# Optimization experiments

Measured on AMD Instinct MI355X. Metric: run time of the kernel, lower is better.

## Reference

```python
import jax, jax.numpy as jnp
import numpy as np

D_MODEL = 1024
STATE_DIM = 64
SEQ_L = 2048


def hippo_legs_A(N):
    n = jnp.arange(N, dtype=jnp.float32)
    two_n1 = 2.0 * n + 1.0
    sq = jnp.sqrt(two_n1[:, None] * two_n1[None, :])
    A = jnp.tril(sq, k=-1) * -1.0
    return A + jnp.diag(-(n + 1.0))


def setup_inputs() -> dict:
    key = jax.random.key(0)
    kB, kC = jax.random.split(key)
    N = STATE_DIM
    n = jnp.arange(N, dtype=jnp.float32)
    B_ref = jnp.sqrt(2.0 * n + 1.0)  # (N,)
    B = jnp.tile(B_ref[None, :], (D_MODEL, 1)) + 0.01 * jax.random.normal(kB, (D_MODEL, N), dtype=jnp.float32)
    C = 0.1 * jax.random.normal(kC, (D_MODEL, N), dtype=jnp.float32)
    D = jnp.zeros((D_MODEL,), dtype=jnp.float32)
    log_dt = jnp.log(jnp.asarray(0.1, dtype=jnp.float32))
    return {"B": B, "C": C, "D": D, "log_dt": log_dt, "L": SEQ_L}


def reference(B, C, D, log_dt, L):
    N = B.shape[1]
    A = hippo_legs_A(N)                       # (N,N) continuous-time HiPPO-LegS
    dt = jax.nn.softplus(log_dt) + 1e-06
    I = jnp.eye(N, dtype=A.dtype)
    lhs = I - 0.5 * dt * A
    rhs = I + 0.5 * dt * A
    A_bar = jnp.linalg.solve(lhs, rhs)        # (N,N) bilinear discretization
    B_bar = jnp.linalg.solve(lhs, (dt * B).T).T  # (d_model, N)
    A_bar_T = A_bar.T

    def step(x, _):
        y = jnp.sum(C * x, axis=-1)           # (d_model,)
        return x @ A_bar_T, y

    _, ys = jax.lax.scan(step, B_bar, None, length=L)  # ys: (L, d_model)
    K = ys.T                                   # (d_model, L)
    K = K.at[:, 0].add(D)
    return K[:, None, :]                       # (d_model, 1, L)
```

## Files before the change

kernel.cpp:

```cpp
#include <hip/hip_runtime.h>

namespace {

template<int CTRL, int RM>
__device__ __forceinline__ float dpp_mov0(float v) {
  return __int_as_float(__builtin_amdgcn_update_dpp(
      0, __float_as_int(v), CTRL, RM, 0xF, false));
}
template<int CTRL, int RM>
__device__ __forceinline__ float dpp_mov1(float v) {
  return __int_as_float(__builtin_amdgcn_update_dpp(
      0x3f800000, __float_as_int(v), CTRL, RM, 0xF, false));
}

struct Hoist {
  float cs0, cs1, cs2, cs3, cs4, cs5;
  float gs0, gs1, gs2, gs3, gs4, gs5;
  float r, inv_d, hr, alpha, k2;
};

__device__ __forceinline__ Hoist make_hoist(float dt, int n) {
  float h = 0.5f * dt, fn = (float)n;
  float r = sqrtf(2.f * fn + 1.f);
  float d = 1.f + h * (fn + 1.f);
  float inv_d = 1.f / d;
  float g = (1.f - h * fn) * inv_d;
  float c = g - 1.f;
  Hoist H;
  H.r = r; H.inv_d = inv_d; H.hr = h * r;
  H.alpha = 1.f + h * fn;
  H.k2 = r * (2.f - d) * inv_d;
#define COEF_STEP(IDX, CTRL, RM)                                        \
  H.cs##IDX = c; H.gs##IDX = g;                                         \
  { float cP = dpp_mov0<CTRL, RM>(c);                                   \
    float gP = dpp_mov1<CTRL, RM>(g);                                   \
    c = fmaf(g, cP, c); g = g * gP; }
  COEF_STEP(0, 0x111, 0xF)
  COEF_STEP(1, 0x112, 0xF)
  COEF_STEP(2, 0x114, 0xF)
  COEF_STEP(3, 0x118, 0xF)
  COEF_STEP(4, 0x142, 0xA)
  COEF_STEP(5, 0x143, 0xC)
#undef COEF_STEP
  return H;
}

__device__ __forceinline__ float abar_apply(float x, const Hoist& H) {
  float w1 = H.r * x, w2 = H.k2 * x;
#define APPLY_STEP(IDX, CTRL, RM)                                       \
  { float w1P = dpp_mov0<CTRL, RM>(w1);                                 \
    float w2P = dpp_mov0<CTRL, RM>(w2);                                 \
    w2 = fmaf(H.cs##IDX, w1P, fmaf(H.gs##IDX, w2P, w2));                \
    w1 += w1P; }
  APPLY_STEP(0, 0x111, 0xF)
  APPLY_STEP(1, 0x112, 0xF)
  APPLY_STEP(2, 0x114, 0xF)
  APPLY_STEP(3, 0x118, 0xF)
  APPLY_STEP(4, 0x142, 0xA)
  APPLY_STEP(5, 0x143, 0xC)
#undef APPLY_STEP
  float tp = dpp_mov0<0x138, 0xF>(w2);
  return H.inv_d * fmaf(-H.hr, w1 + tp, H.alpha * x);
}

template<int CTRL, int RM>
__device__ __forceinline__ void linrec_step(float& G, float& W) {
  float Wo = dpp_mov0<CTRL, RM>(W);
  float Go = dpp_mov1<CTRL, RM>(G);
  W = fmaf(G, Wo, W);
  G *= Go;
}
__device__ __forceinline__ float lhs_solve(float z, const Hoist& H) {
  float G = H.gs0, W = H.r * z * H.inv_d;
  linrec_step<0x111, 0xF>(G, W);
  linrec_step<0x112, 0xF>(G, W);
  linrec_step<0x114, 0xF>(G, W);
  linrec_step<0x118, 0xF>(G, W);
  linrec_step<0x142, 0xA>(G, W);
  linrec_step<0x143, 0xC>(G, W);
  float sp = dpp_mov0<0x138, 0xF>(W);
  return (z - H.hr * sp) * H.inv_d;
}

__device__ __forceinline__ float softplus_dt(float ldt) {
  return log1pf(expf(ldt)) + 1e-6f;
}

__device__ __forceinline__ void load_row(const float* __restrict__ base,
                                         float (&pc)[64]) {
  const float4* p4 = (const float4*)base;
  #pragma unroll
  for (int q = 0; q < 16; ++q) {
    float4 f = p4[q];
    pc[4*q+0] = f.x; pc[4*q+1] = f.y; pc[4*q+2] = f.z; pc[4*q+3] = f.w;
  }
}

__device__ __forceinline__ float qapply(const float (&pc)[64], float u) {
  float a0 = 0.f, a1 = 0.f, a2 = 0.f, a3 = 0.f;
  #pragma unroll
  for (int k = 0; k < 64; k += 4) {
    float u0 = __int_as_float(__builtin_amdgcn_readlane(__float_as_int(u), k + 0));
    float u1 = __int_as_float(__builtin_amdgcn_readlane(__float_as_int(u), k + 1));
    float u2 = __int_as_float(__builtin_amdgcn_readlane(__float_as_int(u), k + 2));
    float u3 = __int_as_float(__builtin_amdgcn_readlane(__float_as_int(u), k + 3));
    a0 = fmaf(pc[k + 0], u0, a0);
    a1 = fmaf(pc[k + 1], u1, a1);
    a2 = fmaf(pc[k + 2], u2, a2);
    a3 = fmaf(pc[k + 3], u3, a3);
  }
  return (a0 + a1) + (a2 + a3);
}

__device__ __forceinline__ float lds_matvec(const float (&pc)[64],
                                            const float* row) {
  const float4* r4 = (const float4*)row;
  float a0 = 0.f, a1 = 0.f, a2 = 0.f, a3 = 0.f;
  #pragma unroll
  for (int q = 0; q < 16; ++q) {
    float4 f = r4[q];
    a0 = fmaf(pc[4*q+0], f.x, a0);
    a1 = fmaf(pc[4*q+1], f.y, a1);
    a2 = fmaf(pc[4*q+2], f.z, a2);
    a3 = fmaf(pc[4*q+3], f.w, a3);
  }
  return (a0 + a1) + (a2 + a3);
}

}

__global__ __launch_bounds__(64) void hippo_pow(const float* __restrict__ ldt_p,
                                                float* __restrict__ A32c,
                                                float* __restrict__ QROW,
                                                float* __restrict__ Q2ROW) {
  const int lane = threadIdx.x;
  const int m = blockIdx.x;
  const float dt = softplus_dt(ldt_p[0]);
  const Hoist H = make_hoist(dt, lane);
  float x = (lane == m) ? 1.f : 0.f;
  #pragma unroll 1
  for (int s = 0; s < 32; ++s) x = abar_apply(x, H);
  A32c[lane * 64 + m] = x;
  #pragma unroll 1
  for (int s = 0; s < 32; ++s) x = abar_apply(x, H);
  QROW[m * 64 + lane] = x;
  #pragma unroll 1
  for (int s = 0; s < 64; ++s) x = abar_apply(x, H);
  Q2ROW[m * 64 + lane] = x;
}

__global__ __launch_bounds__(256, 4) void hippo_main(
    const float* __restrict__ B, const float* __restrict__ C,
    const float* __restrict__ Dv, const float* __restrict__ ldt_p,
    const float* __restrict__ A32c, const float* __restrict__ QROW,
    const float* __restrict__ Q2ROW, float* __restrict__ out, int NI, int L) {
  __shared__ __align__(16) float Vl[64 * 65];
  __shared__ __align__(16) float Ul[32 * 64];
  const int d = blockIdx.x;
  const int tau = threadIdx.x;
  const int lane = tau & 63;
  const int w = tau >> 6;
  const float dt = softplus_dt(ldt_p[0]);
  const Hoist H = make_hoist(dt, lane);

  if (w == 0) {
    float v = lhs_solve(dt * B[d * 64 + lane], H);
    #pragma unroll 1
    for (int j = 0; j < 32; ++j) {
      Vl[j * 65 + lane] = v;
      if (j < 31) v = abar_apply(v, H);
    }
  } else if (w == 3) {
    float bb = lhs_solve(dt * B[d * 64 + lane], H);
    float pc[64];
    load_row(A32c + lane * 64, pc);
    float v = qapply(pc, bb);
    #pragma unroll 1
    for (int j = 32; j < 64; ++j) {
      Vl[j * 65 + lane] = v;
      if (j < 63) v = abar_apply(v, H);
    }
  } else if (w == 1) {
    float pc[64];
    load_row(Q2ROW + lane * 64, pc);
    float u = C[d * 64 + lane];
    const int nE = (NI + 1) >> 1;
    #pragma unroll 1
    for (int a = 0; a < nE; ++a) {
      Ul[(2 * a) * 64 + lane] = u;
      if (a < nE - 1) u = lds_matvec(pc, Ul + (2 * a) * 64);
    }
  } else {
    float pc[64];
    load_row(QROW + lane * 64, pc);
    float u = qapply(pc, C[d * 64 + lane]);
    load_row(Q2ROW + lane * 64, pc);
    const int nO = NI >> 1;
    #pragma unroll 1
    for (int a = 0; a < nO; ++a) {
      Ul[(2 * a + 1) * 64 + lane] = u;
      if (a < nO - 1) u = lds_matvec(pc, Ul + (2 * a + 1) * 64);
    }
  }
  __syncthreads();

  const int j = lane;
  float vr[64];
  #pragma unroll
  for (int n = 0; n < 64; ++n) vr[n] = Vl[j * 65 + n];
  #pragma unroll
  for (int k = 0; k < 8; ++k) {
    const int i = w + 4 * k;
    if (i < NI) {
      const float4* u4 = (const float4*)(Ul + i * 64);
      float a0 = 0.f, a1 = 0.f, a2 = 0.f, a3 = 0.f;
      #pragma unroll
      for (int q = 0; q < 16; ++q) {
        float4 f = u4[q];
        a0 = fmaf(vr[4*q+0], f.x, a0);
        a1 = fmaf(vr[4*q+1], f.y, a1);
        a2 = fmaf(vr[4*q+2], f.z, a2);
        a3 = fmaf(vr[4*q+3], f.w, a3);
      }
      float y = (a0 + a1) + (a2 + a3);
      if ((i | j) == 0) y += Dv[d];
      out[(size_t)d * L + i * 64 + j] = y;
    }
  }
}

extern "C" void kernel_launch(void* const* d_in, const int* in_sizes, int n_in,
                              void* d_out, int out_size, void* d_ws, size_t ws_size,
                              hipStream_t stream) {
  const float* B   = (const float*)d_in[0];
  const float* C   = (const float*)d_in[1];
  const float* Dv  = (const float*)d_in[2];
  const float* ldt = (const float*)d_in[3];
  const int d_model = in_sizes[2];
  const int L = out_size / d_model;
  const int NI = L / 64;
  float* A32c  = (float*)d_ws;
  float* QROW  = (float*)d_ws + 4096;
  float* Q2ROW = (float*)d_ws + 8192;
  hippo_pow<<<64, 64, 0, stream>>>(ldt, A32c, QROW, Q2ROW);
  hippo_main<<<d_model, 256, 0, stream>>>(B, C, Dv, ldt, A32c, QROW, Q2ROW,
                                          (float*)d_out, NI, L);
}
```

Before: 44.79 us.

## Cut register pressure in hippo_main by streaming matrices from LDS and global memory

Replaces the 64-register row caches (pc[64], vr[64]) with on-the-fly matvecs: the A32c and QROW products read rows from global memory and broadcast the input with readlane. The Q2 recurrence now reads a transposed copy staged in shared memory. The final V·U contraction is split into four 16-wide chunks with per-output accumulators. V storage switches from 65-column padding to an XOR swizzle. The aim is lower VGPR use so the 4-blocks-per-CU launch bound holds without spills, at the cost of extra LDS traffic per recurrence step, a serial accumulation order, and a larger shared footprint.

```diff
diff --git a/kernel.cpp b/kernel.cpp
--- a/kernel.cpp
+++ b/kernel.cpp
@@ -11,6 +11,10 @@
 __device__ __forceinline__ float dpp_mov1(float v) {
   return __int_as_float(__builtin_amdgcn_update_dpp(
       0x3f800000, __float_as_int(v), CTRL, RM, 0xF, false));
+}
+
+__device__ __forceinline__ float rl(float v, int k) {
+  return __int_as_float(__builtin_amdgcn_readlane(__float_as_int(v), k));
 }
 
 struct Hoist {
@@ -86,43 +90,33 @@
   return log1pf(expf(ldt)) + 1e-6f;
 }
 
-__device__ __forceinline__ void load_row(const float* __restrict__ base,
-                                         float (&pc)[64]) {
-  const float4* p4 = (const float4*)base;
+__device__ __forceinline__ float grow_matvec(const float* __restrict__ M,
+                                             float u, int lane) {
+  float a0 = 0.f, a1 = 0.f, a2 = 0.f, a3 = 0.f;
+  const float4* m4 = (const float4*)(M + lane * 64);
   #pragma unroll
   for (int q = 0; q < 16; ++q) {
-    float4 f = p4[q];
-    pc[4*q+0] = f.x; pc[4*q+1] = f.y; pc[4*q+2] = f.z; pc[4*q+3] = f.w;
-  }
-}
-
-__device__ __forceinline__ float qapply(const float (&pc)[64], float u) {
+    float4 f = m4[q];
+    a0 = fmaf(f.x, rl(u, 4 * q + 0), a0);
+    a1 = fmaf(f.y, rl(u, 4 * q + 1), a1);
+    a2 = fmaf(f.z, rl(u, 4 * q + 2), a2);
+    a3 = fmaf(f.w, rl(u, 4 * q + 3), a3);
+  }
+  return (a0 + a1) + (a2 + a3);
+}
+
+__device__ __forceinline__ float q2t_matvec(const float* Q2T, float u, int lane) {
   float a0 = 0.f, a1 = 0.f, a2 = 0.f, a3 = 0.f;
   #pragma unroll
   for (int k = 0; k < 64; k += 4) {
-    float u0 = __int_as_float(__builtin_amdgcn_readlane(__float_as_int(u), k + 0));
-    float u1 = __int_as_float(__builtin_amdgcn_readlane(__float_as_int(u), k + 1));
-    float u2 = __int_as_float(__builtin_amdgcn_readlane(__float_as_int(u), k + 2));
-    float u3 = __int_as_float(__builtin_amdgcn_readlane(__float_as_int(u), k + 3));
-    a0 = fmaf(pc[k + 0], u0, a0);
-    a1 = fmaf(pc[k + 1], u1, a1);
-    a2 = fmaf(pc[k + 2], u2, a2);
-    a3 = fmaf(pc[k + 3], u3, a3);
-  }
-  return (a0 + a1) + (a2 + a3);
-}
-
-__device__ __forceinline__ float lds_matvec(const float (&pc)[64],
-                                            const float* row) {
-  const float4* r4 = (const float4*)row;
-  float a0 = 0.f, a1 = 0.f, a2 = 0.f, a3 = 0.f;
-  #pragma unroll
-  for (int q = 0; q < 16; ++q) {
-    float4 f = r4[q];
-    a0 = fmaf(pc[4*q+0], f.x, a0);
-    a1 = fmaf(pc[4*q+1], f.y, a1);
-    a2 = fmaf(pc[4*q+2], f.z, a2);
-    a3 = fmaf(pc[4*q+3], f.w, a3);
+    float q0 = Q2T[(k + 0) * 64 + lane];
+    float q1 = Q2T[(k + 1) * 64 + lane];
+    float q2 = Q2T[(k + 2) * 64 + lane];
+    float q3 = Q2T[(k + 3) * 64 + lane];
+    a0 = fmaf(q0, rl(u, k + 0), a0);
+    a1 = fmaf(q1, rl(u, k + 1), a1);
+    a2 = fmaf(q2, rl(u, k + 2), a2);
+    a3 = fmaf(q3, rl(u, k + 3), a3);
   }
   return (a0 + a1) + (a2 + a3);
 }
@@ -154,75 +148,100 @@
     const float* __restrict__ Dv, const float* __restrict__ ldt_p,
     const float* __restrict__ A32c, const float* __restrict__ QROW,
     const float* __restrict__ Q2ROW, float* __restrict__ out, int NI, int L) {
-  __shared__ __align__(16) float Vl[64 * 65];
+  __shared__ __align__(16) float Vl[64 * 64];
   __shared__ __align__(16) float Ul[32 * 64];
+  __shared__ __align__(16) float Q2T[64 * 64];
   const int d = blockIdx.x;
   const int tau = threadIdx.x;
   const int lane = tau & 63;
   const int w = tau >> 6;
-  const float dt = softplus_dt(ldt_p[0]);
-  const Hoist H = make_hoist(dt, lane);
 
   if (w == 0) {
-    float v = lhs_solve(dt * B[d * 64 + lane], H);
+    const Hoist H = make_hoist(softplus_dt(ldt_p[0]), lane);
+    float v = lhs_solve(softplus_dt(ldt_p[0]) * B[d * 64 + lane], H);
     #pragma unroll 1
     for (int j = 0; j < 32; ++j) {
-      Vl[j * 65 + lane] = v;
+      Vl[j * 64 + (lane ^ (j & 31))] = v;
       if (j < 31) v = abar_apply(v, H);
     }
   } else if (w == 3) {
-    float bb = lhs_solve(dt * B[d * 64 + lane], H);
-    float pc[64];
-    load_row(A32c + lane * 64, pc);
-    float v = qapply(pc, bb);
+    const Hoist H = make_hoist(softplus_dt(ldt_p[0]), lane);
+    float bb = lhs_solve(softplus_dt(ldt_p[0]) * B[d * 64 + lane], H);
+    float v = grow_matvec(A32c, bb, lane);
     #pragma unroll 1
     for (int j = 32; j < 64; ++j) {
-      Vl[j * 65 + lane] = v;
+      Vl[j * 64 + (lane ^ (j & 31))] = v;
       if (j < 63) v = abar_apply(v, H);
     }
-  } else if (w == 1) {
-    float pc[64];
-    load_row(Q2ROW + lane * 64, pc);
-    float u = C[d * 64 + lane];
-    const int nE = (NI + 1) >> 1;
-    #pragma unroll 1
-    for (int a = 0; a < nE; ++a) {
-      Ul[(2 * a) * 64 + lane] = u;
-      if (a < nE - 1) u = lds_matvec(pc, Ul + (2 * a) * 64);
-    }
   } else {
-    float pc[64];
-    load_row(QROW + lane * 64, pc);
-    float u = qapply(pc, C[d * 64 + lane]);
-    load_row(Q2ROW + lane * 64, pc);
-    const int nO = NI >> 1;
-    #pragma unroll 1
-    for (int a = 0; a < nO; ++a) {
-      Ul[(2 * a + 1) * 64 + lane] = u;
-      if (a < nO - 1) u = lds_matvec(pc, Ul + (2 * a + 1) * 64);
+    #pragma unroll
+    for (int q = 0; q < 16; ++q) {
+      float4 f = *(const float4*)(Q2ROW + lane * 64 + 4 * q);
+      Q2T[(4 * q + 0) * 64 + lane] = f.x;
+      Q2T[(4 * q + 1) * 64 + lane] = f.y;
+      Q2T[(4 * q + 2) * 64 + lane] = f.z;
+      Q2T[(4 * q + 3) * 64 + lane] = f.w;
+    }
+    if (w == 1) {
+      float u = C[d * 64 + lane];
+      const int nE = (NI + 1) >> 1;
+      #pragma unroll 1
+      for (int a = 0; a < nE; ++a) {
+        Ul[(2 * a) * 64 + lane] = u;
+        if (a < nE - 1) u = q2t_matvec(Q2T, u, lane);
+      }
+    } else {
+      float u = grow_matvec(QROW, C[d * 64 + lane], lane);
+      const int nO = NI >> 1;
+      #pragma unroll 1
+      for (int a = 0; a < nO; ++a) {
+        Ul[(2 * a + 1) * 64 + lane] = u;
+        if (a < nO - 1) u = q2t_matvec(Q2T, u, lane);
+      }
     }
   }
   __syncthreads();
 
   const int j = lane;
-  float vr[64];
-  #pragma unroll
-  for (int n = 0; n < 64; ++n) vr[n] = Vl[j * 65 + n];
+  float acc[8];
+  #pragma unroll
+  for (int k = 0; k < 8; ++k) acc[k] = 0.f;
+  #pragma unroll
+  for (int h = 0; h < 4; ++h) {
+    float vr[16];
+    #pragma unroll
+    for (int e = 0; e < 16; ++e)
+      vr[e] = Vl[j * 64 + ((16 * h + e) ^ (j & 31))];
+    #pragma unroll
+    for (int k = 0; k < 8; ++k) {
+      const int i = w + 4 * k;
+      if (i < NI) {
+        const float4* u4 = (const float4*)(Ul + i * 64 + 16 * h);
+        float4 f0 = u4[0], f1 = u4[1], f2 = u4[2], f3 = u4[3];
+        acc[k] = fmaf(vr[0],  f0.x, acc[k]);
+        acc[k] = fmaf(vr[1],  f0.y, acc[k]);
+        acc[k] = fmaf(vr[2],  f0.z, acc[k]);
+        acc[k] = fmaf(vr[3],  f0.w, acc[k]);
+        acc[k] = fmaf(vr[4],  f1.x, acc[k]);
+        acc[k] = fmaf(vr[5],  f1.y, acc[k]);
+        acc[k] = fmaf(vr[6],  f1.z, acc[k]);
+        acc[k] = fmaf(vr[7],  f1.w, acc[k]);
+        acc[k] = fmaf(vr[8],  f2.x, acc[k]);
+        acc[k] = fmaf(vr[9],  f2.y, acc[k]);
+        acc[k] = fmaf(vr[10], f2.z, acc[k]);
+        acc[k] = fmaf(vr[11], f2.w, acc[k]);
+        acc[k] = fmaf(vr[12], f3.x, acc[k]);
+        acc[k] = fmaf(vr[13], f3.y, acc[k]);
+        acc[k] = fmaf(vr[14], f3.z, acc[k]);
+        acc[k] = fmaf(vr[15], f3.w, acc[k]);
+      }
+    }
+  }
   #pragma unroll
   for (int k = 0; k < 8; ++k) {
     const int i = w + 4 * k;
     if (i < NI) {
-      const float4* u4 = (const float4*)(Ul + i * 64);
-      float a0 = 0.f, a1 = 0.f, a2 = 0.f, a3 = 0.f;
-      #pragma unroll
-      for (int q = 0; q < 16; ++q) {
-        float4 f = u4[q];
-        a0 = fmaf(vr[4*q+0], f.x, a0);
-        a1 = fmaf(vr[4*q+1], f.y, a1);
-        a2 = fmaf(vr[4*q+2], f.z, a2);
-        a3 = fmaf(vr[4*q+3], f.w, a3);
-      }
-      float y = (a0 + a1) + (a2 + a3);
+      float y = acc[k];
       if ((i | j) == 0) y += Dv[d];
       out[(size_t)d * L + i * 64 + j] = y;
     }
```

Result: no change. 45.57 us (+1.7%).
